# Performance work log

Hardware: AMD Instinct MI355X
Metric: run time of the kernel (lower is better)

The kernel has to match this reference:

```python
import jax, jax.numpy as jnp
import numpy as np

S = 8192   # seq_len (== max_seq_len)
K = 4096   # in_features
N = 4096   # out_features


def setup_inputs() -> dict:
    key = jax.random.key(0)
    k1, k2, k3, k4, k5 = jax.random.split(key, 5)
    # symmetric int8 activations and weights in [-127, 127]
    x = jax.random.randint(k1, (S, K), -127, 128, dtype=jnp.int32).astype(jnp.int8)
    weight_q = jax.random.randint(k2, (N, K), -127, 128, dtype=jnp.int32).astype(jnp.int8)
    # positive dequant scales (per-row symmetric quant: scale = absmax/127)
    scale_x = jax.random.uniform(k3, (S,), minval=0.5, maxval=2.0, dtype=jnp.float32) / 127.0
    scale_w = jax.random.uniform(k4, (N,), minval=0.5, maxval=2.0, dtype=jnp.float32) / 127.0
    # per-output-row requantization scale from the MinMax observer
    scale_y = jax.random.uniform(k5, (S,), minval=0.5, maxval=2.0, dtype=jnp.float32)
    return {"x": x, "weight_q": weight_q, "scale_x": scale_x,
            "scale_w": scale_w, "scale_y": scale_y}


def reference(x, weight_q, scale_x, scale_w, scale_y):
    # int8 GEMM with int32 accumulation: acc[s, n] = sum_k x[s, k] * w[n, k]
    acc = jnp.matmul(x.astype(jnp.int32), weight_q.T.astype(jnp.int32))  # [S, N] int32
    # fused three-scale dequant + requant: (acc * sx[s] * sw[n]) / sy[s]
    scale = (scale_x / scale_y)[:, None] * scale_w[None, :]               # [S, N]
    out_f = acc.astype(jnp.float32) * scale
    out_q = jnp.clip(jnp.round(out_f), -128.0, 127.0).astype(jnp.int8)    # int8 output
    return out_q, scale_y
```

## Files before the change

### kernel.cpp

```cpp
#include <hip/hip_runtime.h>
#include <stdint.h>

#define S_DIM 8192
#define K_DIM 4096
#define N_DIM 4096

#define BM 128
#define BN 256
#define BK 128

typedef int v4i __attribute__((ext_vector_type(4)));

__global__ void prep(const int* __restrict__ x, const int* __restrict__ w,
                     const float* __restrict__ sy,
                     int* __restrict__ dst, float* __restrict__ out) {
    const int nx = S_DIM * K_DIM / 4;
    const int nw = N_DIM * K_DIM / 4;
    int i = blockIdx.x * 256 + threadIdx.x;
    if (i < nx) {
        int4 a = ((const int4*)x)[i];
        dst[i] = (a.x & 0xFF) | ((a.y & 0xFF) << 8) | ((a.z & 0xFF) << 16)
               | ((a.w & 0xFF) << 24);
    } else if (i < nx + nw) {
        int4 a = ((const int4*)w)[i - nx];
        dst[i] = (a.x & 0xFF) | ((a.y & 0xFF) << 8) | ((a.z & 0xFF) << 16)
               | ((a.w & 0xFF) << 24);
    } else {
        int j = i - nx - nw;
        if (j < S_DIM) out[(size_t)S_DIM * N_DIM + j] = sy[j];
    }
}

__global__ void copy_sy(const float* __restrict__ sy, float* __restrict__ out) {
    int i = blockIdx.x * blockDim.x + threadIdx.x;
    if (i < S_DIM) out[(size_t)S_DIM * N_DIM + i] = sy[i];
}

__device__ __forceinline__ void g2lds16(const void* g, void* l) {
    __builtin_amdgcn_global_load_lds((const __attribute__((address_space(1))) void*)g,
                                     (__attribute__((address_space(3))) void*)l,
                                     16, 0, 0);
}

__launch_bounds__(256, 2)
__global__ void gemm_i8(const signed char* __restrict__ xp,
                        const signed char* __restrict__ wp,
                        const float* __restrict__ sx,
                        const float* __restrict__ sw,
                        const float* __restrict__ sy,
                        float* __restrict__ out) {
    __shared__ __align__(16) signed char As[BM * BK];
    __shared__ __align__(16) signed char Bs[BN * BK];

    const int tid  = threadIdx.x;
    const int lane = tid & 63;
    const int quad = lane >> 4;
    const int l16  = lane & 15;
    const int wave = tid >> 6;
    const int wm = wave >> 1;
    const int wn = wave & 1;
    const int bn = blockIdx.x;
    const int bm = blockIdx.y;

    const signed char* aG = xp + (size_t)(bm * BM) * K_DIM;
    const signed char* bG = wp + (size_t)(bn * BN) * K_DIM;

    const int csw = l16 & 7;

    int aOff[4], bOff[8];
#pragma unroll
    for (int i = 0; i < 4; i++) {
        int li = i * 256 + tid;
        int row = li >> 3, c = li & 7, g = c ^ (row & 7);
        aOff[i] = row * K_DIM + (g << 4);
    }
#pragma unroll
    for (int i = 0; i < 8; i++) {
        int li = i * 256 + tid;
        int row = li >> 3, c = li & 7, g = c ^ (row & 7);
        bOff[i] = row * K_DIM + (g << 4);
    }

    v4i acc[4][8];
#pragma unroll
    for (int i = 0; i < 4; i++)
#pragma unroll
        for (int j = 0; j < 8; j++) acc[i][j] = 0;

    for (int kk = 0; kk < K_DIM; kk += BK) {
        __syncthreads();
#pragma unroll
        for (int i = 0; i < 4; i++)
            g2lds16(aG + aOff[i] + kk, As + (i * 256 + tid) * 16);
#pragma unroll
        for (int i = 0; i < 8; i++)
            g2lds16(bG + bOff[i] + kk, Bs + (i * 256 + tid) * 16);
        __syncthreads();

#pragma unroll
        for (int ks = 0; ks < 2; ks++) {
            const int slot = ((ks << 2) | quad) ^ csw;
            v4i af[4], bf[8];
#pragma unroll
            for (int t = 0; t < 4; t++)
                af[t] = *(const v4i*)(As + (wm * 64 + t * 16 + l16) * BK
                                         + (slot << 4));
#pragma unroll
            for (int u = 0; u < 8; u++)
                bf[u] = *(const v4i*)(Bs + (wn * 128 + u * 16 + l16) * BK
                                         + (slot << 4));
#pragma unroll
            for (int mt = 0; mt < 4; mt++)
#pragma unroll
                for (int nt = 0; nt < 8; nt++)
                    acc[mt][nt] = __builtin_amdgcn_mfma_i32_16x16x64_i8(
                        af[mt], bf[nt], acc[mt][nt], 0, 0, 0);
        }
    }

    const int s_base = bm * BM + wm * 64;
    const int n_base = bn * BN + wn * 128;
#pragma unroll
    for (int mt = 0; mt < 4; mt++) {
#pragma unroll
        for (int r = 0; r < 4; r++) {
            int s = s_base + mt * 16 + quad * 4 + r;
            float rs = sx[s] / sy[s];
            float* orow = out + (size_t)s * N_DIM;
#pragma unroll
            for (int nt = 0; nt < 8; nt++) {
                int n = n_base + nt * 16 + l16;
                float v = rintf((float)acc[mt][nt][r] * (rs * sw[n]));
                v = fminf(fmaxf(v, -128.f), 127.f);
                orow[n] = v;
            }
        }
    }
}

__global__ void gemm_naive(const int* __restrict__ x, const int* __restrict__ w,
                           const float* __restrict__ sx, const float* __restrict__ sw,
                           const float* __restrict__ sy, float* __restrict__ out) {
    int n = blockIdx.x * blockDim.x + threadIdx.x;
    int s = blockIdx.y;
    const int4* xr = (const int4*)(x + (size_t)s * K_DIM);
    const int4* wr = (const int4*)(w + (size_t)n * K_DIM);
    int acc = 0;
    for (int k = 0; k < K_DIM / 4; k++) {
        int4 a = xr[k], b = wr[k];
        acc += a.x * b.x + a.y * b.y + a.z * b.z + a.w * b.w;
    }
    float v = rintf((float)acc * (sx[s] / sy[s] * sw[n]));
    out[(size_t)s * N_DIM + n] = fminf(fmaxf(v, -128.f), 127.f);
}

extern "C" void kernel_launch(void* const* d_in, const int* in_sizes, int n_in,
                              void* d_out, int out_size, void* d_ws, size_t ws_size,
                              hipStream_t stream) {
    const int*   x  = (const int*)d_in[0];
    const int*   wq = (const int*)d_in[1];
    const float* sx = (const float*)d_in[2];
    const float* sw = (const float*)d_in[3];
    const float* sy = (const float*)d_in[4];
    float* out = (float*)d_out;

    const size_t need = (size_t)S_DIM * K_DIM + (size_t)N_DIM * K_DIM;
    if (ws_size >= need) {
        signed char* xp = (signed char*)d_ws;
        signed char* wp = xp + (size_t)S_DIM * K_DIM;
        const int nprep = (S_DIM * K_DIM / 4) + (N_DIM * K_DIM / 4) + S_DIM;
        prep<<<dim3((nprep + 255) / 256), dim3(256), 0, stream>>>(
            x, wq, sy, (int*)xp, out);
        gemm_i8<<<dim3(N_DIM / BN, S_DIM / BM), dim3(256), 0, stream>>>(
            xp, wp, sx, sw, sy, out);
    } else {
        copy_sy<<<dim3((S_DIM + 255) / 256), dim3(256), 0, stream>>>(sy, out);
        gemm_naive<<<dim3(N_DIM / 256, S_DIM), dim3(256), 0, stream>>>(
            x, wq, sx, sw, sy, out);
    }
}
```

Measured before the change: 380.1 us.

## Restructure int8 GEMM into 256x256 tiles with 4-stage async LDS pipeline

Grows the block tile to 256x256 with 512 threads (8 waves, 2x4) and shrinks the K step to 64. It adds a 4-deep ring of LDS buffers filled by direct global-to-LDS loads issued three tiles ahead, and splits each K step into two MFMA halves with explicit vmcnt/lgkmcnt waits, barriers and setprio. The goal is to hide global memory latency behind MFMA work and to raise arithmetic intensity per loaded byte. In exchange it needs more LDS (128KB per block, which may limit occupancy) and relies on hand-tuned waitcnt counts that must match the issue order.

```diff
diff --git a/kernel.cpp b/kernel.cpp
--- a/kernel.cpp
+++ b/kernel.cpp
@@ -5,9 +5,10 @@
 #define K_DIM 4096
 #define N_DIM 4096
 
-#define BM 128
+#define BM 256
 #define BN 256
-#define BK 128
+#define BKB 64
+#define NT (K_DIM / BKB)
 
 typedef int v4i __attribute__((ext_vector_type(4)));
 
@@ -42,95 +43,128 @@
                                      16, 0, 0);
 }
 
-__launch_bounds__(256, 2)
+__launch_bounds__(512, 2)
 __global__ void gemm_i8(const signed char* __restrict__ xp,
                         const signed char* __restrict__ wp,
                         const float* __restrict__ sx,
                         const float* __restrict__ sw,
                         const float* __restrict__ sy,
                         float* __restrict__ out) {
-    __shared__ __align__(16) signed char As[BM * BK];
-    __shared__ __align__(16) signed char Bs[BN * BK];
+    __shared__ __align__(16) signed char As[4][BM * BKB];
+    __shared__ __align__(16) signed char Bs[4][BN * BKB];
 
     const int tid  = threadIdx.x;
     const int lane = tid & 63;
     const int quad = lane >> 4;
     const int l16  = lane & 15;
     const int wave = tid >> 6;
-    const int wm = wave >> 1;
-    const int wn = wave & 1;
+    const int wm = wave >> 2;
+    const int wn = wave & 3;
     const int bn = blockIdx.x;
     const int bm = blockIdx.y;
 
     const signed char* aG = xp + (size_t)(bm * BM) * K_DIM;
     const signed char* bG = wp + (size_t)(bn * BN) * K_DIM;
 
-    const int csw = l16 & 7;
-
-    int aOff[4], bOff[8];
-#pragma unroll
-    for (int i = 0; i < 4; i++) {
-        int li = i * 256 + tid;
-        int row = li >> 3, c = li & 7, g = c ^ (row & 7);
-        aOff[i] = row * K_DIM + (g << 4);
-    }
-#pragma unroll
-    for (int i = 0; i < 8; i++) {
-        int li = i * 256 + tid;
-        int row = li >> 3, c = li & 7, g = c ^ (row & 7);
-        bOff[i] = row * K_DIM + (g << 4);
-    }
-
-    v4i acc[4][8];
-#pragma unroll
-    for (int i = 0; i < 4; i++)
-#pragma unroll
-        for (int j = 0; j < 8; j++) acc[i][j] = 0;
-
-    for (int kk = 0; kk < K_DIM; kk += BK) {
-        __syncthreads();
-#pragma unroll
-        for (int i = 0; i < 4; i++)
-            g2lds16(aG + aOff[i] + kk, As + (i * 256 + tid) * 16);
-#pragma unroll
-        for (int i = 0; i < 8; i++)
-            g2lds16(bG + bOff[i] + kk, Bs + (i * 256 + tid) * 16);
-        __syncthreads();
-
-#pragma unroll
-        for (int ks = 0; ks < 2; ks++) {
-            const int slot = ((ks << 2) | quad) ^ csw;
-            v4i af[4], bf[8];
-#pragma unroll
-            for (int t = 0; t < 4; t++)
-                af[t] = *(const v4i*)(As + (wm * 64 + t * 16 + l16) * BK
-                                         + (slot << 4));
-#pragma unroll
-            for (int u = 0; u < 8; u++)
-                bf[u] = *(const v4i*)(Bs + (wn * 128 + u * 16 + l16) * BK
-                                         + (slot << 4));
-#pragma unroll
-            for (int mt = 0; mt < 4; mt++)
-#pragma unroll
-                for (int nt = 0; nt < 8; nt++)
-                    acc[mt][nt] = __builtin_amdgcn_mfma_i32_16x16x64_i8(
-                        af[mt], bf[nt], acc[mt][nt], 0, 0, 0);
-        }
-    }
-
-    const int s_base = bm * BM + wm * 64;
-    const int n_base = bn * BN + wn * 128;
-#pragma unroll
-    for (int mt = 0; mt < 4; mt++) {
+    int gOff0, gOff1;
+    {
+        int L = tid;
+        int s = L >> 3, sl = L & 7, p = sl ^ (s & 7);
+        gOff0 = (2 * s + (p >> 2)) * K_DIM + ((p & 3) << 4);
+        L = 512 + tid;
+        s = L >> 3; sl = L & 7; p = sl ^ (s & 7);
+        gOff1 = (2 * s + (p >> 2)) * K_DIM + ((p & 3) << 4);
+    }
+
+    const int rdo = ((l16 >> 1) * 128)
+                  + (((((l16 & 1) << 2) | quad) ^ ((l16 >> 1) & 7)) << 4);
+
+#define STAGE_A(T) do { const int kk_ = (T) * BKB;                          \
+        signed char* d_ = &As[(T) & 3][0];                                  \
+        g2lds16(aG + gOff0 + kk_, d_ + tid * 16);                           \
+        g2lds16(aG + gOff1 + kk_, d_ + 8192 + tid * 16); } while (0)
+#define STAGE_B(T) do { const int kk_ = (T) * BKB;                          \
+        signed char* d_ = &Bs[(T) & 3][0];                                  \
+        g2lds16(bG + gOff0 + kk_, d_ + tid * 16);                           \
+        g2lds16(bG + gOff1 + kk_, d_ + 8192 + tid * 16); } while (0)
+
+    v4i acc[8][4];
+#pragma unroll
+    for (int i = 0; i < 8; i++)
+#pragma unroll
+        for (int j = 0; j < 4; j++) acc[i][j] = 0;
+
+    STAGE_A(0); STAGE_B(0);
+    STAGE_A(1); STAGE_B(1);
+    STAGE_A(2); STAGE_B(2);
+    asm volatile("s_waitcnt vmcnt(8)" ::: "memory");
+    __builtin_amdgcn_s_barrier();
+
+    for (int t = 0; t < NT; ++t) {
+        const signed char* a_lds = &As[t & 3][0] + wm * (128 * 64) + rdo;
+        const signed char* b_lds = &Bs[t & 3][0] + wn * (64 * 64) + rdo;
+
+        v4i a0[4], bf[4];
+#pragma unroll
+        for (int mt = 0; mt < 4; mt++)
+            a0[mt] = *(const v4i*)(a_lds + mt * 1024);
+#pragma unroll
+        for (int nt = 0; nt < 4; nt++)
+            bf[nt] = *(const v4i*)(b_lds + nt * 1024);
+        if (t + 3 < NT) STAGE_A(t + 3);
+        __builtin_amdgcn_s_barrier();
+        asm volatile("s_waitcnt lgkmcnt(0)" ::: "memory");
+        __builtin_amdgcn_sched_barrier(0);
+        __builtin_amdgcn_s_setprio(1);
+#pragma unroll
+        for (int mt = 0; mt < 4; mt++)
+#pragma unroll
+            for (int nt = 0; nt < 4; nt++)
+                acc[mt][nt] = __builtin_amdgcn_mfma_i32_16x16x64_i8(
+                    a0[mt], bf[nt], acc[mt][nt], 0, 0, 0);
+        __builtin_amdgcn_s_setprio(0);
+        __builtin_amdgcn_s_barrier();
+
+        v4i a1[4];
+#pragma unroll
+        for (int mt = 0; mt < 4; mt++)
+            a1[mt] = *(const v4i*)(a_lds + (4 + mt) * 1024);
+        if (t + 3 < NT) STAGE_B(t + 3);
+        if (t < NT - 3)       asm volatile("s_waitcnt vmcnt(8)" ::: "memory");
+        else if (t == NT - 3) asm volatile("s_waitcnt vmcnt(4)" ::: "memory");
+        else                  asm volatile("s_waitcnt vmcnt(0)" ::: "memory");
+        __builtin_amdgcn_s_barrier();
+        asm volatile("s_waitcnt lgkmcnt(0)" ::: "memory");
+        __builtin_amdgcn_sched_barrier(0);
+        __builtin_amdgcn_s_setprio(1);
+#pragma unroll
+        for (int mt = 0; mt < 4; mt++)
+#pragma unroll
+            for (int nt = 0; nt < 4; nt++)
+                acc[4 + mt][nt] = __builtin_amdgcn_mfma_i32_16x16x64_i8(
+                    a1[mt], bf[nt], acc[4 + mt][nt], 0, 0, 0);
+        __builtin_amdgcn_s_setprio(0);
+        __builtin_amdgcn_s_barrier();
+    }
+#undef STAGE_A
+#undef STAGE_B
+
+    const int s_base = bm * BM + wm * 128;
+    const int n_base = bn * BN + wn * 64;
+    float swv[4];
+#pragma unroll
+    for (int nt = 0; nt < 4; nt++) swv[nt] = sw[n_base + nt * 16 + l16];
+#pragma unroll
+    for (int mt = 0; mt < 8; mt++) {
 #pragma unroll
         for (int r = 0; r < 4; r++) {
             int s = s_base + mt * 16 + quad * 4 + r;
             float rs = sx[s] / sy[s];
             float* orow = out + (size_t)s * N_DIM;
 #pragma unroll
-            for (int nt = 0; nt < 8; nt++) {
+            for (int nt = 0; nt < 4; nt++) {
                 int n = n_base + nt * 16 + l16;
-                float v = rintf((float)acc[mt][nt][r] * (rs * sw[n]));
+                float v = rintf((float)acc[mt][nt][r] * (rs * swv[nt]));
                 v = fminf(fmaxf(v, -128.f), 127.f);
                 orow[n] = v;
             }
@@ -171,7 +205,7 @@
         const int nprep = (S_DIM * K_DIM / 4) + (N_DIM * K_DIM / 4) + S_DIM;
         prep<<<dim3((nprep + 255) / 256), dim3(256), 0, stream>>>(
             x, wq, sy, (int*)xp, out);
-        gemm_i8<<<dim3(N_DIM / BN, S_DIM / BM), dim3(256), 0, stream>>>(
+        gemm_i8<<<dim3(N_DIM / BN, S_DIM / BM), dim3(512), 0, stream>>>(
             xp, wp, sx, sw, sy, out);
     } else {
         copy_sy<<<dim3((S_DIM + 255) / 256), dim3(256), 0, stream>>>(sy, out);
```

Result: slower. 393.0 us (+3.4%).

## Triple-buffer LDS tiles with async global-to-LDS prefetch two stages ahead

Applied to the files above, without the earlier changes.

Splits K into 64-byte tiles and keeps three LDS buffers. Loads for tile t+2 are issued while tile t is computed, and explicit vmcnt waits plus raw barriers replace the full syncthreads pair. The LDS layout is repacked with two rows per 128-byte line and a new XOR swizzle for conflict-free fragment reads. This is meant to hide global load latency behind MFMA work, at the cost of more LDS per block and fragile hand-tuned wait counts.

```diff
diff --git a/kernel.cpp b/kernel.cpp
--- a/kernel.cpp
+++ b/kernel.cpp
@@ -7,7 +7,9 @@
 
 #define BM 128
 #define BN 256
-#define BK 128
+#define BKB 64
+#define NT (K_DIM / BKB)
+#define RD 3
 
 typedef int v4i __attribute__((ext_vector_type(4)));
 
@@ -49,8 +51,8 @@
                         const float* __restrict__ sw,
                         const float* __restrict__ sy,
                         float* __restrict__ out) {
-    __shared__ __align__(16) signed char As[BM * BK];
-    __shared__ __align__(16) signed char Bs[BN * BK];
+    __shared__ __align__(16) signed char As[RD][BM * BKB];
+    __shared__ __align__(16) signed char Bs[RD][BN * BKB];
 
     const int tid  = threadIdx.x;
     const int lane = tid & 63;
@@ -65,21 +67,33 @@
     const signed char* aG = xp + (size_t)(bm * BM) * K_DIM;
     const signed char* bG = wp + (size_t)(bn * BN) * K_DIM;
 
-    const int csw = l16 & 7;
-
-    int aOff[4], bOff[8];
+    int aOff[2], bOff[4];
+#pragma unroll
+    for (int i = 0; i < 2; i++) {
+        int L = i * 256 + tid;
+        int s = L >> 3, p = (L & 7) ^ (s & 7);
+        aOff[i] = (2 * s + (p >> 2)) * K_DIM + ((p & 3) << 4);
+    }
 #pragma unroll
     for (int i = 0; i < 4; i++) {
-        int li = i * 256 + tid;
-        int row = li >> 3, c = li & 7, g = c ^ (row & 7);
-        aOff[i] = row * K_DIM + (g << 4);
-    }
-#pragma unroll
-    for (int i = 0; i < 8; i++) {
-        int li = i * 256 + tid;
-        int row = li >> 3, c = li & 7, g = c ^ (row & 7);
-        bOff[i] = row * K_DIM + (g << 4);
-    }
+        int L = i * 256 + tid;
+        int s = L >> 3, p = (L & 7) ^ (s & 7);
+        bOff[i] = (2 * s + (p >> 2)) * K_DIM + ((p & 3) << 4);
+    }
+
+    const int rdo = ((l16 >> 1) * 128)
+                  + (((((l16 & 1) << 2) | quad) ^ (l16 >> 1)) << 4);
+
+#define STAGE(T, SL) do { const int kk_ = (T) * BKB;                        \
+        signed char* da_ = &As[SL][0];                                      \
+        signed char* db_ = &Bs[SL][0];                                      \
+        g2lds16(aG + aOff[0] + kk_, da_ + tid * 16);                        \
+        g2lds16(aG + aOff[1] + kk_, da_ + 4096 + tid * 16);                 \
+        g2lds16(bG + bOff[0] + kk_, db_ + tid * 16);                        \
+        g2lds16(bG + bOff[1] + kk_, db_ + 4096 + tid * 16);                 \
+        g2lds16(bG + bOff[2] + kk_, db_ + 8192 + tid * 16);                 \
+        g2lds16(bG + bOff[3] + kk_, db_ + 12288 + tid * 16);                \
+    } while (0)
 
     v4i acc[4][8];
 #pragma unroll
@@ -87,36 +101,41 @@
 #pragma unroll
         for (int j = 0; j < 8; j++) acc[i][j] = 0;
 
-    for (int kk = 0; kk < K_DIM; kk += BK) {
-        __syncthreads();
-#pragma unroll
-        for (int i = 0; i < 4; i++)
-            g2lds16(aG + aOff[i] + kk, As + (i * 256 + tid) * 16);
-#pragma unroll
-        for (int i = 0; i < 8; i++)
-            g2lds16(bG + bOff[i] + kk, Bs + (i * 256 + tid) * 16);
-        __syncthreads();
-
-#pragma unroll
-        for (int ks = 0; ks < 2; ks++) {
-            const int slot = ((ks << 2) | quad) ^ csw;
-            v4i af[4], bf[8];
-#pragma unroll
-            for (int t = 0; t < 4; t++)
-                af[t] = *(const v4i*)(As + (wm * 64 + t * 16 + l16) * BK
-                                         + (slot << 4));
-#pragma unroll
-            for (int u = 0; u < 8; u++)
-                bf[u] = *(const v4i*)(Bs + (wn * 128 + u * 16 + l16) * BK
-                                         + (slot << 4));
-#pragma unroll
-            for (int mt = 0; mt < 4; mt++)
-#pragma unroll
-                for (int nt = 0; nt < 8; nt++)
-                    acc[mt][nt] = __builtin_amdgcn_mfma_i32_16x16x64_i8(
-                        af[mt], bf[nt], acc[mt][nt], 0, 0, 0);
-        }
-    }
+    STAGE(0, 0);
+    STAGE(1, 1);
+
+    int cs = 0;
+    for (int t = 0; t < NT; ++t) {
+        __builtin_amdgcn_s_barrier();
+        __builtin_amdgcn_sched_barrier(0);
+        int ns = cs + 2; if (ns >= RD) ns -= RD;
+        if (t + 2 < NT) STAGE(t + 2, ns);
+        __builtin_amdgcn_sched_barrier(0);
+        if (t < NT - 2)       asm volatile("s_waitcnt vmcnt(12)" ::: "memory");
+        else if (t == NT - 2) asm volatile("s_waitcnt vmcnt(6)" ::: "memory");
+        else                  asm volatile("s_waitcnt vmcnt(0)" ::: "memory");
+        __builtin_amdgcn_s_barrier();
+        __builtin_amdgcn_sched_barrier(0);
+
+        const signed char* a_lds = &As[cs][0] + wm * 4096 + rdo;
+        const signed char* b_lds = &Bs[cs][0] + wn * 8192 + rdo;
+        v4i af[4], bf[8];
+#pragma unroll
+        for (int mt = 0; mt < 4; mt++)
+            af[mt] = *(const v4i*)(a_lds + mt * 1024);
+#pragma unroll
+        for (int nt = 0; nt < 8; nt++)
+            bf[nt] = *(const v4i*)(b_lds + nt * 1024);
+#pragma unroll
+        for (int mt = 0; mt < 4; mt++)
+#pragma unroll
+            for (int nt = 0; nt < 8; nt++)
+                acc[mt][nt] = __builtin_amdgcn_mfma_i32_16x16x64_i8(
+                    af[mt], bf[nt], acc[mt][nt], 0, 0, 0);
+
+        cs++; if (cs >= RD) cs = 0;
+    }
+#undef STAGE
 
     const int s_base = bm * BM + wm * 64;
     const int n_base = bn * BN + wn * 128;
```

After: 407.7 us. 7.3% more time.

## Switch int8 GEMM to 32x32x32 MFMA with double-buffered LDS fragment loads

Applied to the files above, without the earlier changes.

Replaces the 16x16x64 int8 MFMA tiling (4x8 tiles per wave) with 32x32x32 MFMA tiles (2x4 per wave), so each wave issues fewer, larger matrix instructions and reads fewer LDS fragments per k-step. Fragment reads from LDS are software-pipelined across four k-substeps so the next fragment loads overlap the current MFMAs. The epilogue is remapped to the 32x32 output layout and hoists the per-column scale_w loads. The larger tile changes the register footprint and the LDS read pattern against the existing XOR swizzle, which may introduce bank conflicts or register pressure.

```diff
diff --git a/kernel.cpp b/kernel.cpp
--- a/kernel.cpp
+++ b/kernel.cpp
@@ -9,7 +9,8 @@
 #define BN 256
 #define BK 128
 
-typedef int v4i __attribute__((ext_vector_type(4)));
+typedef int v4i  __attribute__((ext_vector_type(4)));
+typedef int v16i __attribute__((ext_vector_type(16)));
 
 __global__ void prep(const int* __restrict__ x, const int* __restrict__ w,
                      const float* __restrict__ sy,
@@ -54,8 +55,9 @@
 
     const int tid  = threadIdx.x;
     const int lane = tid & 63;
-    const int quad = lane >> 4;
-    const int l16  = lane & 15;
+    const int r32  = lane & 31;
+    const int h    = lane >> 5;
+    const int c7   = lane & 7;
     const int wave = tid >> 6;
     const int wm = wave >> 1;
     const int wn = wave & 1;
@@ -65,8 +67,6 @@
     const signed char* aG = xp + (size_t)(bm * BM) * K_DIM;
     const signed char* bG = wp + (size_t)(bn * BN) * K_DIM;
 
-    const int csw = l16 & 7;
-
     int aOff[4], bOff[8];
 #pragma unroll
     for (int i = 0; i < 4; i++) {
@@ -81,11 +81,23 @@
         bOff[i] = row * K_DIM + (g << 4);
     }
 
-    v4i acc[4][8];
-#pragma unroll
-    for (int i = 0; i < 4; i++)
-#pragma unroll
-        for (int j = 0; j < 8; j++) acc[i][j] = 0;
+    int o[4];
+#pragma unroll
+    for (int ks = 0; ks < 4; ks++)
+        o[ks] = ((((ks << 1) | h) ^ c7) << 4);
+
+    const signed char* aB0 = As + (wm * 64 +  0 + r32) * BK;
+    const signed char* aB1 = As + (wm * 64 + 32 + r32) * BK;
+    const signed char* bB0 = Bs + (wn * 128 +  0 + r32) * BK;
+    const signed char* bB1 = Bs + (wn * 128 + 32 + r32) * BK;
+    const signed char* bB2 = Bs + (wn * 128 + 64 + r32) * BK;
+    const signed char* bB3 = Bs + (wn * 128 + 96 + r32) * BK;
+
+    v16i acc[2][4];
+#pragma unroll
+    for (int i = 0; i < 2; i++)
+#pragma unroll
+        for (int j = 0; j < 4; j++) acc[i][j] = 0;
 
     for (int kk = 0; kk < K_DIM; kk += BK) {
         __syncthreads();
@@ -97,42 +109,55 @@
             g2lds16(bG + bOff[i] + kk, Bs + (i * 256 + tid) * 16);
         __syncthreads();
 
-#pragma unroll
-        for (int ks = 0; ks < 2; ks++) {
-            const int slot = ((ks << 2) | quad) ^ csw;
-            v4i af[4], bf[8];
-#pragma unroll
-            for (int t = 0; t < 4; t++)
-                af[t] = *(const v4i*)(As + (wm * 64 + t * 16 + l16) * BK
-                                         + (slot << 4));
-#pragma unroll
-            for (int u = 0; u < 8; u++)
-                bf[u] = *(const v4i*)(Bs + (wn * 128 + u * 16 + l16) * BK
-                                         + (slot << 4));
-#pragma unroll
-            for (int mt = 0; mt < 4; mt++)
-#pragma unroll
-                for (int nt = 0; nt < 8; nt++)
-                    acc[mt][nt] = __builtin_amdgcn_mfma_i32_16x16x64_i8(
-                        af[mt], bf[nt], acc[mt][nt], 0, 0, 0);
+        v4i af[2][2], bf[2][4];
+        af[0][0] = *(const v4i*)(aB0 + o[0]);
+        af[0][1] = *(const v4i*)(aB1 + o[0]);
+        bf[0][0] = *(const v4i*)(bB0 + o[0]);
+        bf[0][1] = *(const v4i*)(bB1 + o[0]);
+        bf[0][2] = *(const v4i*)(bB2 + o[0]);
+        bf[0][3] = *(const v4i*)(bB3 + o[0]);
+#pragma unroll
+        for (int ks = 0; ks < 4; ks++) {
+            const int cur = ks & 1, nxt = cur ^ 1;
+            if (ks < 3) {
+                af[nxt][0] = *(const v4i*)(aB0 + o[ks + 1]);
+                af[nxt][1] = *(const v4i*)(aB1 + o[ks + 1]);
+                bf[nxt][0] = *(const v4i*)(bB0 + o[ks + 1]);
+                bf[nxt][1] = *(const v4i*)(bB1 + o[ks + 1]);
+                bf[nxt][2] = *(const v4i*)(bB2 + o[ks + 1]);
+                bf[nxt][3] = *(const v4i*)(bB3 + o[ks + 1]);
+            }
+#pragma unroll
+            for (int mt = 0; mt < 2; mt++)
+#pragma unroll
+                for (int nt = 0; nt < 4; nt++)
+                    acc[mt][nt] = __builtin_amdgcn_mfma_i32_32x32x32_i8(
+                        af[cur][mt], bf[cur][nt], acc[mt][nt], 0, 0, 0);
         }
     }
 
     const int s_base = bm * BM + wm * 64;
     const int n_base = bn * BN + wn * 128;
-#pragma unroll
-    for (int mt = 0; mt < 4; mt++) {
-#pragma unroll
-        for (int r = 0; r < 4; r++) {
-            int s = s_base + mt * 16 + quad * 4 + r;
-            float rs = sx[s] / sy[s];
-            float* orow = out + (size_t)s * N_DIM;
-#pragma unroll
-            for (int nt = 0; nt < 8; nt++) {
-                int n = n_base + nt * 16 + l16;
-                float v = rintf((float)acc[mt][nt][r] * (rs * sw[n]));
-                v = fminf(fmaxf(v, -128.f), 127.f);
-                orow[n] = v;
+    float swv[4];
+#pragma unroll
+    for (int nt = 0; nt < 4; nt++) swv[nt] = sw[n_base + nt * 32 + r32];
+#pragma unroll
+    for (int mt = 0; mt < 2; mt++) {
+#pragma unroll
+        for (int q = 0; q < 4; q++) {
+#pragma unroll
+            for (int rr = 0; rr < 4; rr++) {
+                int s = s_base + mt * 32 + q * 8 + h * 4 + rr;
+                float rs = sx[s] / sy[s];
+                float* orow = out + (size_t)s * N_DIM;
+#pragma unroll
+                for (int nt = 0; nt < 4; nt++) {
+                    int n = n_base + nt * 32 + r32;
+                    float v = rintf((float)acc[mt][nt][q * 4 + rr]
+                                    * (rs * swv[nt]));
+                    v = fminf(fmaxf(v, -128.f), 127.f);
+                    orow[n] = v;
+                }
             }
         }
     }
```

Result: slower. 403.8 us (+6.2%).
